# Kernel tuning notes

Hardware: AMD Instinct MI355X
Metric: run time of the kernel (lower is better)

The kernel has to match this reference:

```python
import jax, jax.numpy as jnp
import numpy as np

N_NODES = 50000


def _gcn_conv(h, W, b, src, dst, dinv):
    # PyG GCNConv: linear transform, then symmetric-normalized sum aggregation
    h = h @ W  # (N, d_out)
    norm = dinv[src] * dinv[dst]  # (E,)
    msg = h[src] * norm[:, None]  # (E, d_out)
    agg = jax.ops.segment_sum(msg, dst, num_segments=N_NODES)
    return agg + b


def setup_inputs() -> dict:
    key = jax.random.key(0)
    ks = jax.random.split(key, 9)
    in_dim, h1, h2, out_dim = 512, 512, 512, 256
    x = jax.random.normal(ks[0], (N_NODES, in_dim), dtype=jnp.float32)
    edge_index = jax.random.randint(ks[1], (2, 800000), 0, N_NODES, dtype=jnp.int64)

    def glorot(k, shape):
        lim = float(np.sqrt(6.0 / (shape[0] + shape[1])))
        return jax.random.uniform(k, shape, jnp.float32, -lim, lim)

    return {
        "x": x,
        "edge_index": edge_index,
        "W1": glorot(ks[2], (in_dim, h1)),
        "b1": jnp.zeros((h1,), jnp.float32),
        "W2": glorot(ks[3], (h1, h2)),
        "b2": jnp.zeros((h2,), jnp.float32),
        "Wout": glorot(ks[4], (h2, out_dim)),
        "bout": jnp.zeros((out_dim,), jnp.float32),
    }


def reference(x, edge_index, W1, b1, W2, b2, Wout, bout):
    # add self-loops (GCNConv default)
    loop = jnp.arange(N_NODES, dtype=edge_index.dtype)
    src = jnp.concatenate([edge_index[0], loop])
    dst = jnp.concatenate([edge_index[1], loop])
    # degree on A + I (target side), deg^{-1/2}
    deg = jax.ops.segment_sum(jnp.ones_like(dst, dtype=x.dtype), dst, num_segments=N_NODES)
    dinv = jnp.where(deg > 0, jax.lax.rsqrt(deg), 0.0)

    h = jax.nn.relu(_gcn_conv(x, W1, b1, src, dst, dinv))
    h = jax.nn.relu(_gcn_conv(h, W2, b2, src, dst, dinv))
    return h @ Wout + bout
```

## Files before the change

### kernel.cpp

```cpp
#include <hip/hip_runtime.h>

#define NN 50000
#define MP 50176
#define DD 512
#define EE 800000
#define NSCAN 196
#define SCB 3321
#define CNTB 3125
#define WTB 2560
#define CVB 25088
#define CSRTOT (EE + NN + 3 * NN + 64)

typedef unsigned short u16;
typedef __attribute__((ext_vector_type(4))) float f32x4;
typedef __attribute__((ext_vector_type(8))) __bf16 bf16x8;
typedef __attribute__((ext_vector_type(8))) short s16x8;
typedef __attribute__((ext_vector_type(4))) short s16x4;

typedef __attribute__((address_space(1))) const void GVoid;
typedef __attribute__((address_space(3))) void LVoid;

__device__ __forceinline__ u16 f2bf(float f) {
  union { float f; unsigned u; } x; x.f = f;
  unsigned r = x.u + 0x7fffu + ((x.u >> 16) & 1u);
  return (u16)(r >> 16);
}
__device__ __forceinline__ float bf2f(u16 b) {
  union { unsigned u; float f; } x; x.u = ((unsigned)b) << 16;
  return x.f;
}


__global__ __launch_bounds__(256) void count_k(const int* __restrict__ dst, int* __restrict__ cnt) {
  int e = (int)blockIdx.x * 256 + threadIdx.x;
  atomicAdd(&cnt[dst[e]], 1);
}


__global__ __launch_bounds__(256) void scan1_k(const int* __restrict__ cnt, int* __restrict__ bsum) {
  __shared__ int s[256];
  const int t = threadIdx.x;
  const int i = blockIdx.x * 256 + t;
  s[t] = (i < NN) ? ((cnt[i] + 1 + 3) & ~3) : 0;
  __syncthreads();
  for (int off = 128; off > 0; off >>= 1) {
    if (t < off) s[t] += s[t + off];
    __syncthreads();
  }
  if (t == 0) bsum[blockIdx.x] = s[0];
}

__global__ __launch_bounds__(256) void scan2_k(const int* __restrict__ bsum, int* __restrict__ boff) {
  __shared__ int s[256];
  const int t = threadIdx.x;
  const int v = (t < NSCAN) ? bsum[t] : 0;
  s[t] = v;
  __syncthreads();
  for (int off = 1; off < 256; off <<= 1) {
    int a = s[t];
    int b = (t >= off) ? s[t - off] : 0;
    __syncthreads();
    s[t] = a + b;
    __syncthreads();
  }
  if (t < NSCAN) boff[t] = s[t] - v;
}

__global__ __launch_bounds__(256) void scan3_k(const int* __restrict__ cnt, const int* __restrict__ boff,
                                               int* __restrict__ rowp, int* __restrict__ cursor,
                                               float* __restrict__ dinv) {
  __shared__ int s[256];
  const int t = threadIdx.x;
  const int i = blockIdx.x * 256 + t;
  const int v = (i < NN) ? (cnt[i] + 1) : 0;
  const int pv = (v + 3) & ~3;
  s[t] = pv;
  __syncthreads();
  for (int off = 1; off < 256; off <<= 1) {
    int a = s[t];
    int b = (t >= off) ? s[t - off] : 0;
    __syncthreads();
    s[t] = a + b;
    __syncthreads();
  }
  const int excl = s[t] - pv + boff[blockIdx.x];
  if (i < NN) {
    rowp[i] = excl; cursor[i] = excl;
    dinv[i] = rsqrtf((float)v);
  }
  if (i == NN - 1) rowp[NN] = excl + pv;
}


__global__ __launch_bounds__(256) void scatgat_k(const int* __restrict__ src, const int* __restrict__ dst,
                                                 const float* __restrict__ dinv, int* __restrict__ cursor,
                                                 int2* __restrict__ csr,
                                                 const float* __restrict__ W1, u16* __restrict__ W1T,
                                                 const float* __restrict__ W2, u16* __restrict__ W2T,
                                                 const float* __restrict__ Wo, u16* __restrict__ WoT,
                                                 const float* __restrict__ x, u16* __restrict__ xb) {
  const int b = (int)blockIdx.x, t = threadIdx.x;
  if (b < SCB) {
    int e = b * 256 + t;
    if (e < EE) {
      int d = dst[e], sn = src[e];
      int pos = atomicAdd(&cursor[d], 1);
      csr[pos] = make_int2(sn << 10, __float_as_int(dinv[sn] * dinv[d]));
    } else if (e < EE + NN) {
      int i = e - EE;
      int pos = atomicAdd(&cursor[i], 1);
      float di = dinv[i];
      csr[pos] = make_int2(i << 10, __float_as_int(di * di));
    }
    return;
  }
  if (b < SCB + WTB) {
    int b0 = b - SCB;
    int idx, k, n;
    if (b0 < 1024)      { idx = b0 * 256 + t;          k = idx >> 9; n = idx & 511; W1T[n * 512 + k] = f2bf(W1[idx]); }
    else if (b0 < 2048) { idx = (b0 - 1024) * 256 + t; k = idx >> 9; n = idx & 511; W2T[n * 512 + k] = f2bf(W2[idx]); }
    else                { idx = (b0 - 2048) * 256 + t; k = idx >> 8; n = idx & 255; WoT[n * 512 + k] = f2bf(Wo[idx]); }
    return;
  }
  size_t i = ((size_t)(b - SCB - WTB) * 256 + t) * 4;
  if (i >= (size_t)MP * DD) return;
  s16x4 v;
  if (i < (size_t)NN * DD) {
    f32x4 f = *(const f32x4*)(x + i);
    v = (s16x4){ (short)f2bf(f.x), (short)f2bf(f.y), (short)f2bf(f.z), (short)f2bf(f.w) };
  } else {
    v = (s16x4){ 0, 0, 0, 0 };
  }
  *(s16x4*)(xb + i) = v;
}


template<int OUT_BF16>
__global__ __launch_bounds__(512) void gemm256_k(const u16* __restrict__ A, const u16* __restrict__ BT,
                                                 void* __restrict__ Cv, const float* __restrict__ bias,
                                                 int M, int N) {
  const int nwg = (int)gridDim.x;
  const int id = (int)blockIdx.x;
  const int xcd = id & 7;
  const int idx = id >> 3;
  const int q = nwg >> 3;
  const int tile = xcd * q + idx;
  const int ntn = N >> 7;
  const int bm = tile / ntn;
  const int bn = tile % ntn;

  __shared__ u16 As[2][256 * 32];
  __shared__ u16 Bs[2][128 * 32];
  const int t = threadIdx.x;
  const int lane = t & 63;
  const int wid = t >> 6;
  const int wm = wid >> 1;
  const int wn = wid & 1;
  f32x4 acc[4][4] = {};
  const int r0 = t >> 2;
  const int kc = (t & 3) * 8;
  const u16* Ab = A + (size_t)bm * 256 * DD + (size_t)r0 * DD + kc;
  const u16* Bb = BT + (size_t)bn * 128 * DD + (size_t)r0 * DD + kc;

  auto stage = [&](int buf, int kt) {
    __builtin_amdgcn_global_load_lds((GVoid*)(Ab + kt),            (LVoid*)(&As[buf][t * 8]),        16, 0, 0);
    __builtin_amdgcn_global_load_lds((GVoid*)(Ab + 128 * DD + kt), (LVoid*)(&As[buf][4096 + t * 8]), 16, 0, 0);
    __builtin_amdgcn_global_load_lds((GVoid*)(Bb + kt),            (LVoid*)(&Bs[buf][t * 8]),        16, 0, 0);
  };

  stage(0, 0);
  __syncthreads();

  #pragma unroll 2
  for (int step = 0; step < 16; ++step) {
    const int cur = step & 1;
    if (step < 15) stage(cur ^ 1, (step + 1) * 32);
    bf16x8 af[4], bv[4];
    #pragma unroll
    for (int m = 0; m < 4; ++m)
      af[m] = *(const bf16x8*)&As[cur][(wm * 64 + m * 16 + (lane & 15)) * 32 + (lane >> 4) * 8];
    #pragma unroll
    for (int n = 0; n < 4; ++n)
      bv[n] = *(const bf16x8*)&Bs[cur][(wn * 64 + n * 16 + (lane & 15)) * 32 + (lane >> 4) * 8];
    #pragma unroll
    for (int m = 0; m < 4; ++m) {
      #pragma unroll
      for (int n = 0; n < 4; ++n)
        acc[m][n] = __builtin_amdgcn_mfma_f32_16x16x32_bf16(af[m], bv[n], acc[m][n], 0, 0, 0);
    }
    __syncthreads();
  }

  const int rb = bm * 256 + wm * 64 + ((lane >> 4) * 4);
  const int cb = bn * 128 + wn * 64 + (lane & 15);
  #pragma unroll
  for (int m = 0; m < 4; ++m) {
    #pragma unroll
    for (int rr = 0; rr < 4; ++rr) {
      const int row = rb + m * 16 + rr;
      if (row < M) {
        #pragma unroll
        for (int n = 0; n < 4; ++n) {
          const int col = cb + n * 16;
          if (OUT_BF16) ((u16*)Cv)[(size_t)row * N + col] = f2bf(acc[m][n][rr]);
          else          ((float*)Cv)[(size_t)row * N + col] = acc[m][n][rr] + bias[col];
        }
      }
    }
  }
}


__global__ __launch_bounds__(256) void aggregate_k(const u16* __restrict__ H, const int* __restrict__ rowp,
                                                   const int2* __restrict__ csr,
                                                   const float* __restrict__ bias,
                                                   u16* __restrict__ out) {
  const int slice = (int)blockIdx.x & 7;
  const int grp = (int)blockIdx.x >> 3;
  const int wid = threadIdx.x >> 6;
  const int lane = threadIdx.x & 63;
  const int g = lane >> 3;
  const int l = lane & 7;
  const int node = grp * 32 + wid * 8 + g;
  if (node >= NN) return;
  const int d0 = slice * 64 + l * 8;
  const int beg = rowp[node];
  const int rounds = (rowp[node + 1] - beg) >> 2;
  const char* Hb = (const char*)H + (size_t)d0 * 2;
  const int4* cp = (const int4*)(csr + beg);
  float a0 = 0.f, a1 = 0.f, a2 = 0.f, a3 = 0.f, a4 = 0.f, a5 = 0.f, a6 = 0.f, a7 = 0.f;

  int4 c01 = cp[0], c23 = cp[1];
  for (int b = 0; b < rounds; ++b) {
    const s16x8 v0 = *(const s16x8*)(Hb + c01.x);
    const s16x8 v1 = *(const s16x8*)(Hb + c01.z);
    const s16x8 v2 = *(const s16x8*)(Hb + c23.x);
    const s16x8 v3 = *(const s16x8*)(Hb + c23.z);
    const int4 n01 = cp[2 * b + 2], n23 = cp[2 * b + 3];
    const float w0 = __int_as_float(c01.y), w1 = __int_as_float(c01.w);
    const float w2 = __int_as_float(c23.y), w3 = __int_as_float(c23.w);
    a0 += bf2f((u16)v0[0]) * w0 + bf2f((u16)v1[0]) * w1 + bf2f((u16)v2[0]) * w2 + bf2f((u16)v3[0]) * w3;
    a1 += bf2f((u16)v0[1]) * w0 + bf2f((u16)v1[1]) * w1 + bf2f((u16)v2[1]) * w2 + bf2f((u16)v3[1]) * w3;
    a2 += bf2f((u16)v0[2]) * w0 + bf2f((u16)v1[2]) * w1 + bf2f((u16)v2[2]) * w2 + bf2f((u16)v3[2]) * w3;
    a3 += bf2f((u16)v0[3]) * w0 + bf2f((u16)v1[3]) * w1 + bf2f((u16)v2[3]) * w2 + bf2f((u16)v3[3]) * w3;
    a4 += bf2f((u16)v0[4]) * w0 + bf2f((u16)v1[4]) * w1 + bf2f((u16)v2[4]) * w2 + bf2f((u16)v3[4]) * w3;
    a5 += bf2f((u16)v0[5]) * w0 + bf2f((u16)v1[5]) * w1 + bf2f((u16)v2[5]) * w2 + bf2f((u16)v3[5]) * w3;
    a6 += bf2f((u16)v0[6]) * w0 + bf2f((u16)v1[6]) * w1 + bf2f((u16)v2[6]) * w2 + bf2f((u16)v3[6]) * w3;
    a7 += bf2f((u16)v0[7]) * w0 + bf2f((u16)v1[7]) * w1 + bf2f((u16)v2[7]) * w2 + bf2f((u16)v3[7]) * w3;
    c01 = n01; c23 = n23;
  }

  s16x8 o;
  o[0] = (short)f2bf(fmaxf(a0 + bias[d0 + 0], 0.f));
  o[1] = (short)f2bf(fmaxf(a1 + bias[d0 + 1], 0.f));
  o[2] = (short)f2bf(fmaxf(a2 + bias[d0 + 2], 0.f));
  o[3] = (short)f2bf(fmaxf(a3 + bias[d0 + 3], 0.f));
  o[4] = (short)f2bf(fmaxf(a4 + bias[d0 + 4], 0.f));
  o[5] = (short)f2bf(fmaxf(a5 + bias[d0 + 5], 0.f));
  o[6] = (short)f2bf(fmaxf(a6 + bias[d0 + 6], 0.f));
  o[7] = (short)f2bf(fmaxf(a7 + bias[d0 + 7], 0.f));
  *(s16x8*)(out + (size_t)node * DD + d0) = o;
}


extern "C" void kernel_launch(void* const* d_in, const int* in_sizes, int n_in,
                              void* d_out, int out_size, void* d_ws, size_t ws_size,
                              hipStream_t stream) {
  const float* x    = (const float*)d_in[0];
  const int*   ei   = (const int*)d_in[1];
  const float* W1   = (const float*)d_in[2];
  const float* b1   = (const float*)d_in[3];
  const float* W2   = (const float*)d_in[4];
  const float* b2   = (const float*)d_in[5];
  const float* Wout = (const float*)d_in[6];
  const float* bout = (const float*)d_in[7];
  float* out = (float*)d_out;
  (void)in_sizes; (void)n_in; (void)out_size; (void)ws_size;

  char* ws = (char*)d_ws;
  size_t off = 0;
  auto alloc = [&](size_t bytes) -> char* {
    char* p = ws + off;
    off = (off + bytes + 255) & ~(size_t)255;
    return p;
  };
  u16*   xb   = (u16*)alloc((size_t)MP * DD * 2);
  u16*   H    = (u16*)alloc((size_t)NN * DD * 2);
  u16*   W1T  = (u16*)alloc(512 * 512 * 2);
  u16*   W2T  = (u16*)alloc(512 * 512 * 2);
  u16*   WoT  = (u16*)alloc(256 * 512 * 2);
  int*   cnt  = (int*)alloc(NN * 4);
  float* dinv = (float*)alloc(NN * 4);
  int*   rowp = (int*)alloc((NN + 1) * 4);
  int*   cur  = (int*)alloc(NN * 4);
  int2*  csr  = (int2*)alloc((size_t)CSRTOT * 8);
  int*   bsum = (int*)alloc(NSCAN * 4);
  int*   boff = (int*)alloc(NSCAN * 4);

  const int* srcp = ei;
  const int* dstp = ei + EE;

  (void)hipMemsetAsync(cnt, 0, NN * 4, stream);
  (void)hipMemsetAsync(csr, 0, (size_t)CSRTOT * 8, stream);

  count_k<<<CNTB, 256, 0, stream>>>(dstp, cnt);
  scan1_k<<<NSCAN, 256, 0, stream>>>(cnt, bsum);
  scan2_k<<<1, 256, 0, stream>>>(bsum, boff);
  scan3_k<<<NSCAN, 256, 0, stream>>>(cnt, boff, rowp, cur, dinv);
  scatgat_k<<<SCB + WTB + CVB, 256, 0, stream>>>(srcp, dstp, dinv, cur, csr,
                                                 W1, W1T, W2, W2T, Wout, WoT, x, xb);

  const int agg_grid = ((NN + 31) / 32) * 8;

  gemm256_k<1><<<(MP / 256) * (512 / 128), 512, 0, stream>>>(xb, W1T, (void*)H, nullptr, NN, 512);
  aggregate_k<<<agg_grid, 256, 0, stream>>>(H, rowp, csr, b1, xb);
  gemm256_k<1><<<(MP / 256) * (512 / 128), 512, 0, stream>>>(xb, W2T, (void*)H, nullptr, NN, 512);
  aggregate_k<<<agg_grid, 256, 0, stream>>>(H, rowp, csr, b2, xb);
  gemm256_k<0><<<(MP / 256) * (256 / 128), 512, 0, stream>>>(xb, WoT, (void*)out, bout, NN, 256);
}
```

Baseline: 420.7 us.

## Add triple-buffered 64-deep-K GEMM with direct global-to-LDS loads for hidden layers

Introduces a new bf16 MFMA GEMM kernel for the two 512x512 hidden-layer transforms. It stages 64-wide K tiles into three LDS buffers via global_load_lds with counted vmcnt waits, so two tiles are in flight while one is computed. It also raises wave priority around the MFMA block and handles uneven XCD tile distribution. The cost targeted is load latency and barrier stalls in the older double-buffered 32-wide-K kernel. In exchange it uses much more LDS (144 KB), which limits it to one workgroup per CU. The epilogue writes scalar bf16 values, which may be less coalesced.

```diff
diff --git a/kernel.cpp b/kernel.cpp
--- a/kernel.cpp
+++ b/kernel.cpp
@@ -135,6 +135,97 @@
 }
 
 
+__global__ __launch_bounds__(512, 1) void gemmp_k(const u16* __restrict__ A, const u16* __restrict__ BT,
+                                                  u16* __restrict__ C, int M, int N) {
+  __shared__ u16 As[3][256 * 64];
+  __shared__ u16 Bs[3][128 * 64];
+  const int nwg = (int)gridDim.x;
+  const int id = (int)blockIdx.x;
+  const int xcd = id & 7;
+  const int idx = id >> 3;
+  const int q = nwg >> 3, r = nwg & 7;
+  const int tile = (xcd < r ? xcd * (q + 1) : r * (q + 1) + (xcd - r) * q) + idx;
+  const int ntn = N >> 7;
+  const int bm = tile / ntn;
+  const int bn = tile % ntn;
+
+  const int t = threadIdx.x;
+  const int lane = t & 63;
+  const int wid = t >> 6;
+  const int wm = wid >> 2;
+  const int wn = wid & 3;
+
+  const u16* Ab = A + (size_t)(bm * 256 + (t >> 3)) * DD + (t & 7) * 8;
+  const u16* Bb = BT + (size_t)(bn * 128 + (t >> 3)) * DD + (t & 7) * 8;
+
+  auto stage = [&](int buf, int kt) {
+    #pragma unroll
+    for (int c = 0; c < 4; ++c)
+      __builtin_amdgcn_global_load_lds((GVoid*)(Ab + (size_t)c * 64 * DD + kt),
+                                       (LVoid*)(&As[buf][c * 4096 + t * 8]), 16, 0, 0);
+    #pragma unroll
+    for (int c = 0; c < 2; ++c)
+      __builtin_amdgcn_global_load_lds((GVoid*)(Bb + (size_t)c * 64 * DD + kt),
+                                       (LVoid*)(&Bs[buf][c * 4096 + t * 8]), 16, 0, 0);
+  };
+
+  const int arow = wm * 128 + (lane & 15);
+  const int acol = (lane >> 4) * 8;
+  const int brow = wn * 32 + (lane & 15);
+
+  f32x4 acc[8][2] = {};
+
+  stage(0, 0);
+  stage(1, 64);
+  asm volatile("s_waitcnt vmcnt(6)" ::: "memory");
+  __builtin_amdgcn_s_barrier();
+
+  #pragma unroll
+  for (int T = 0; T < 8; ++T) {
+    const int buf = T % 3;
+    if (T + 2 < 8) stage((T + 2) % 3, (T + 2) * 64);
+    bf16x8 bfr[2][2];
+    #pragma unroll
+    for (int n = 0; n < 2; ++n)
+      #pragma unroll
+      for (int kk = 0; kk < 2; ++kk)
+        bfr[n][kk] = *(const bf16x8*)&Bs[buf][(brow + n * 16) * 64 + acol + kk * 32];
+    __builtin_amdgcn_s_setprio(1);
+    #pragma unroll
+    for (int m = 0; m < 8; ++m) {
+      const bf16x8 a0 = *(const bf16x8*)&As[buf][(arow + m * 16) * 64 + acol];
+      const bf16x8 a1 = *(const bf16x8*)&As[buf][(arow + m * 16) * 64 + acol + 32];
+      #pragma unroll
+      for (int n = 0; n < 2; ++n) {
+        acc[m][n] = __builtin_amdgcn_mfma_f32_16x16x32_bf16(a0, bfr[n][0], acc[m][n], 0, 0, 0);
+        acc[m][n] = __builtin_amdgcn_mfma_f32_16x16x32_bf16(a1, bfr[n][1], acc[m][n], 0, 0, 0);
+      }
+    }
+    __builtin_amdgcn_s_setprio(0);
+    if (T < 7) {
+      if (T + 2 < 8) asm volatile("s_waitcnt vmcnt(6)" ::: "memory");
+      else           asm volatile("s_waitcnt vmcnt(0)" ::: "memory");
+      __builtin_amdgcn_s_barrier();
+    }
+  }
+
+  const int rb = bm * 256 + wm * 128 + ((lane >> 4) * 4);
+  const int cb = bn * 128 + wn * 32 + (lane & 15);
+  #pragma unroll
+  for (int m = 0; m < 8; ++m) {
+    #pragma unroll
+    for (int rr = 0; rr < 4; ++rr) {
+      const int row = rb + m * 16 + rr;
+      if (row < M) {
+        #pragma unroll
+        for (int n = 0; n < 2; ++n)
+          C[(size_t)row * N + cb + n * 16] = f2bf(acc[m][n][rr]);
+      }
+    }
+  }
+}
+
+
 template<int OUT_BF16>
 __global__ __launch_bounds__(512) void gemm256_k(const u16* __restrict__ A, const u16* __restrict__ BT,
                                                  void* __restrict__ Cv, const float* __restrict__ bias,
@@ -312,9 +403,9 @@
 
   const int agg_grid = ((NN + 31) / 32) * 8;
 
-  gemm256_k<1><<<(MP / 256) * (512 / 128), 512, 0, stream>>>(xb, W1T, (void*)H, nullptr, NN, 512);
+  gemmp_k<<<(MP / 256) * (512 / 128), 512, 0, stream>>>(xb, W1T, H, NN, 512);
   aggregate_k<<<agg_grid, 256, 0, stream>>>(H, rowp, csr, b1, xb);
-  gemm256_k<1><<<(MP / 256) * (512 / 128), 512, 0, stream>>>(xb, W2T, (void*)H, nullptr, NN, 512);
+  gemmp_k<<<(MP / 256) * (512 / 128), 512, 0, stream>>>(xb, W2T, H, NN, 512);
   aggregate_k<<<agg_grid, 256, 0, stream>>>(H, rowp, csr, b2, xb);
   gemm256_k<0><<<(MP / 256) * (256 / 128), 512, 0, stream>>>(xb, WoT, (void*)out, bout, NN, 256);
 }
```

Result: slower. 458.3 us (+8.9%).
